# Performance work log

Measured on AMD Instinct MI355X. Metric: run time of the kernel, lower is better.

## Reference

```python
import jax, jax.numpy as jnp
import numpy as np

N_NODE = 40000  # item vocabulary
H = 100         # hidden size (SR-GNN default)
B = 64          # sessions per batch
L = 16          # items per session (equal-length sessions)
N = B * L       # total graph nodes
E = 2048        # total edges
NL = 1          # GatedGraphConv layers


def setup_inputs() -> dict:
    key = jax.random.key(0)
    ks = jax.random.split(key, 20)
    stdv = 1.0 / np.sqrt(H)
    u = lambda k, shape: jax.random.uniform(k, shape, jnp.float32, -stdv, stdv)
    return {
        "x": jax.random.randint(ks[0], (N,), 0, N_NODE),
        "edge_index": jax.random.randint(ks[1], (2, E), 0, N),
        "edge_weight": jax.random.uniform(ks[2], (E,), jnp.float32),
        "batch": jnp.arange(N) // L,  # node -> session id, equal-length sessions
        "embed": u(ks[3], (N_NODE, H)),
        "ggc_w": u(ks[4], (NL, H, H)),
        "gru_wih": u(ks[5], (3 * H, H)),
        "gru_whh": u(ks[6], (3 * H, H)),
        "gru_bih": u(ks[7], (3 * H,)),
        "gru_bhh": u(ks[8], (3 * H,)),
        "W1_w": u(ks[9], (H, H)), "W1_b": u(ks[10], (H,)),
        "W2_w": u(ks[11], (H, H)), "W2_b": u(ks[12], (H,)),
        "Wt_w": u(ks[13], (H, H)), "Wt_b": u(ks[14], (H,)),
        "q_w": u(ks[15], (1, H)), "q_b": u(ks[16], (1,)),
        "W3_w": u(ks[17], (H, 2 * H)), "W3_b": u(ks[18], (H,)),
    }


def reference(x, edge_index, edge_weight, batch, embed, ggc_w, gru_wih, gru_whh,
              gru_bih, gru_bhh, W1_w, W1_b, W2_w, W2_b, Wt_w, Wt_b, q_w, q_b,
              W3_w, W3_b):
    # Embedding lookup
    h = embed[x]  # [N, H]
    src, dst = edge_index[0], edge_index[1]
    # GatedGraphConv: weighted message aggregation + GRUCell update
    for l in range(NL):
        m = h @ ggc_w[l]                                             # [N, H]
        agg = jnp.zeros_like(h).at[dst].add(edge_weight[:, None] * m[src])
        gi = agg @ gru_wih.T + gru_bih                               # [N, 3H]
        gh = h @ gru_whh.T + gru_bhh
        ir, iz, inn = jnp.split(gi, 3, axis=-1)
        hr, hz, hn = jnp.split(gh, 3, axis=-1)
        r = jax.nn.sigmoid(ir + hr)
        zg = jax.nn.sigmoid(iz + hz)
        ng = jnp.tanh(inn + r * hn)
        h = (1.0 - zg) * ng + zg * h
    v = h.reshape(B, L, H)                                           # sessions
    s_l = v[:, -1]                                                   # [B, H] last item
    # alpha = q(sigmoid(W1(v_n) + W2(v)))
    a = jax.nn.sigmoid((s_l @ W1_w.T + W1_b)[:, None, :] + (v @ W2_w.T + W2_b))
    alpha = a @ q_w.T + q_b                                          # [B, L, 1]
    s_g = jnp.sum(alpha * v, axis=1)                                 # [B, H]
    s_h = jnp.concatenate([s_l, s_g], axis=-1) @ W3_w.T + W3_b       # [B, H]
    # Target attention: s_t[b] = softmax(E @ W_t(v_b)^T, -1) @ v_b, contracted
    # directly against E to avoid materializing [B, N_NODE, H].
    vt = v @ Wt_w.T + Wt_b                                           # [B, L, H]
    P = jax.nn.softmax(jnp.einsum('jh,blh->bjl', embed, vt), axis=-1)
    C = jnp.einsum('blh,jh->bjl', v, embed)                          # v_l . E_j
    z = s_h @ embed.T + jnp.sum(P * C, axis=-1)                      # [B, N_NODE]
    return z
```

## Files before the change

kernel.cpp:

```cpp
#include <hip/hip_runtime.h>
#include <hip/hip_bf16.h>

#define Hh    100
#define NN    1024
#define BB    64
#define LL    16
#define EE    2048
#define NNODE 40000

#define BSPL  8
#define BPB   (BB / BSPL)
#define PFR   8
#define PPAN  (PFR * 64 * 8)
#define GJ    4
#define EBS   104

typedef unsigned short u16;
typedef __attribute__((ext_vector_type(8))) short short8;
typedef __attribute__((ext_vector_type(4))) float f32x4;

__device__ __forceinline__ float bf2f(u16 u) {
    union { unsigned int i; float f; } v;
    v.i = ((unsigned int)u) << 16;
    return v.f;
}

__device__ __forceinline__ u16 f2bf(float f) {
    unsigned int x = __float_as_uint(f);
    unsigned int lsb = (x >> 16) & 1u;
    x += 0x7fffu + lsb;
    return (u16)(x >> 16);
}

__device__ __forceinline__ float sigmoidf_(float x) {
    return 1.0f / (1.0f + expf(-x));
}

template <bool BF>
__device__ __forceinline__ float ldv(const void* p, size_t i) {
    if (BF) return bf2f(((const u16*)p)[i]);
    return ((const float*)p)[i];
}
__device__ __forceinline__ float ldvf(int flag, const void* p, size_t i) {
    return flag ? ldv<true>(p, i) : ldv<false>(p, i);
}

template <bool BF>
__device__ void cvt_impl(int t,
                         const void* ew, const void* ggc, const void* wih, const void* whh,
                         const void* bih, const void* bhh, const void* W1w, const void* W1b,
                         const void* W2w, const void* W2b, const void* Wtw, const void* Wtb,
                         const void* qw, const void* qb, const void* W3w, const void* W3b,
                         float* __restrict__ W) {
    const void* src; int si; int doff; int di;
    if      (t <   2048) { src = ew;  si = t;          doff = 0;      di = si; }
    else if (t <  12048) { src = ggc; si = t - 2048;   doff = 2048;   di = si; }
    else if (t <  42048) { src = wih; si = t - 12048;  doff = 12048;  { int r = si / 100, k = si - r * 100; di = k * 800 + (r % 100) * 8 + r / 100; } }
    else if (t <  72048) { src = whh; si = t - 42048;  doff = 12048;  { int r = si / 100, k = si - r * 100; di = k * 800 + (r % 100) * 8 + 3 + r / 100; } }
    else if (t <  72348) { src = bih; si = t - 72048;  doff = 92048;  di = si; }
    else if (t <  72648) { src = bhh; si = t - 72348;  doff = 92352;  di = si; }
    else if (t <  82648) { src = W1w; si = t - 72648;  doff = 92656;  di = (si % 100) * 100 + si / 100; }
    else if (t <  82748) { src = W1b; si = t - 82648;  doff = 102656; di = si; }
    else if (t <  92748) { src = W2w; si = t - 82748;  doff = 102768; di = (si % 100) * 100 + si / 100; }
    else if (t <  92848) { src = W2b; si = t - 92748;  doff = 112768; di = si; }
    else if (t < 102848) { src = Wtw; si = t - 92848;  doff = 112880; di = (si % 100) * 100 + si / 100; }
    else if (t < 102948) { src = Wtb; si = t - 102848; doff = 122880; di = si; }
    else if (t < 103048) { src = qw;  si = t - 102948; doff = 122992; di = si; }
    else if (t < 103049) { src = qb;  si = t - 103048; doff = 123104; di = si; }
    else if (t < 123049) { src = W3w; si = t - 103049; doff = 123120; di = (si % 200) * 100 + si / 200; }
    else                 { src = W3b; si = t - 123049; doff = 143120; di = si; }
    W[doff + di] = ldv<BF>(src, si);
}

__global__ void __launch_bounds__(256) k_cvt(const void* embed_raw, int* __restrict__ flag,
                      const void* ew, const void* ggc, const void* wih, const void* whh,
                      const void* bih, const void* bhh, const void* W1w, const void* W1b,
                      const void* W2w, const void* W2b, const void* Wtw, const void* Wtb,
                      const void* qw, const void* qb, const void* W3w, const void* W3b,
                      float* __restrict__ W, u16* __restrict__ SD) {
    __shared__ int cnt;
    if (threadIdx.x == 0) cnt = 0;
    __syncthreads();
    int bad = 0;
    const u16* eb = (const u16*)embed_raw;
    for (int i = threadIdx.x; i < 4096; i += 256) {
        float v = bf2f(eb[i]);
        if (!(fabsf(v) <= 0.5f)) bad++;
    }
    if (bad) atomicAdd(&cnt, bad);
    __syncthreads();
    const bool bf = (cnt == 0);
    if (blockIdx.x == 0 && threadIdx.x == 0) flag[0] = bf ? 1 : 0;
    int t = blockIdx.x * 256 + threadIdx.x;
    if (t < 8192) ((unsigned int*)SD)[t] = 0u;
    if (t >= 123149) return;
    if (bf) cvt_impl<true >(t, ew, ggc, wih, whh, bih, bhh, W1w, W1b, W2w, W2b, Wtw, Wtb, qw, qb, W3w, W3b, W);
    else    cvt_impl<false>(t, ew, ggc, wih, whh, bih, bhh, W1w, W1b, W2w, W2b, Wtw, Wtb, qw, qb, W3w, W3b, W);
}

__global__ void __launch_bounds__(256) k_ecvt(const int* __restrict__ flag,
                                              const void* __restrict__ embed,
                                              u16* __restrict__ EB) {
    const bool bf = (flag[0] != 0);
    int t = blockIdx.x * 256 + threadIdx.x;
    const int total = NNODE * (EBS / 2);
    if (t >= total) return;
    int r = t / (EBS / 2), c2 = t - r * (EBS / 2);
    int k0 = c2 * 2;
    unsigned int w = 0;
    if (k0 + 1 < Hh) {
        if (bf) {
            w = *(const unsigned int*)&((const u16*)embed)[(size_t)r * Hh + k0];
        } else {
            float2 e2 = *(const float2*)&((const float*)embed)[(size_t)r * Hh + k0];
            w = (unsigned int)f2bf(e2.x) | ((unsigned int)f2bf(e2.y) << 16);
        }
    }
    ((unsigned int*)EB)[t] = w;
}

__global__ void __launch_bounds__(256) k_gm(const int* __restrict__ flag,
                                            const int* __restrict__ x,
                                            const void* __restrict__ embed,
                                            const float* __restrict__ ggc_w,
                                            float* __restrict__ m,
                                            float* __restrict__ agg) {
    __shared__ float W[Hh * Hh];
    __shared__ float H[8 * Hh];
    const int tid = threadIdx.x;
    const int fl = flag[0];
    const int r0 = blockIdx.x * 8;
    for (int idx = tid; idx < Hh * Hh; idx += 256) W[idx] = ggc_w[idx];
    for (int idx = tid; idx < 8 * Hh; idx += 256) {
        int i = idx / Hh, j = idx - i * Hh;
        H[idx] = ldvf(fl, embed, (size_t)x[r0 + i] * Hh + j);
    }
    for (int idx = tid; idx < 8 * Hh; idx += 256) agg[r0 * Hh + idx] = 0.0f;
    __syncthreads();
    for (int idx = tid; idx < 8 * Hh; idx += 256) {
        int i = idx / Hh, j = idx - i * Hh;
        float acc = 0.0f;
#pragma unroll 4
        for (int k = 0; k < Hh; ++k) acc += H[i * Hh + k] * W[k * Hh + j];
        m[(r0 + i) * Hh + j] = acc;
    }
}

__global__ void k_scatter(const int* __restrict__ ei, const float* __restrict__ ew,
                          const float* __restrict__ m, float* __restrict__ agg) {
    int t = blockIdx.x * 256 + threadIdx.x;
    if (t >= EE * Hh) return;
    int e = t / Hh, j = t - e * Hh;
    int src = ei[e], dst = ei[EE + e];
    atomicAdd(&agg[dst * Hh + j], ew[e] * m[src * Hh + j]);
}

__global__ void k_gru(const int* __restrict__ flag, const int* __restrict__ x,
                      const void* __restrict__ embed,
                      const float* __restrict__ agg,
                      const float* __restrict__ wC,
                      const float* __restrict__ bih, const float* __restrict__ bhh,
                      float* __restrict__ h1) {
    int t = blockIdx.x * 256 + threadIdx.x;
    if (t >= NN * Hh) return;
    int i = t / Hh, j = t - i * Hh;
    const int fl = flag[0];
    const size_t erow = (size_t)x[i] * Hh;
    const float* ar = agg + i * Hh;
    float s_ir = bih[j], s_iz = bih[j + Hh], s_in = bih[j + 2 * Hh];
    float s_hr = bhh[j], s_hz = bhh[j + Hh], s_hn = bhh[j + 2 * Hh];
    float h0j = 0.0f;
    const float* wbase = wC + j * 8;
    for (int k = 0; k < Hh; ++k) {
        float a = ar[k];
        float h = ldvf(fl, embed, erow + k);
        if (k == j) h0j = h;
        const float* wr = wbase + k * 800;
        float4 w0 = *(const float4*)wr;
        float2 w1 = *(const float2*)(wr + 4);
        s_ir += a * w0.x;
        s_iz += a * w0.y;
        s_in += a * w0.z;
        s_hr += h * w0.w;
        s_hz += h * w1.x;
        s_hn += h * w1.y;
    }
    float r = sigmoidf_(s_ir + s_hr);
    float z = sigmoidf_(s_iz + s_hz);
    float n = tanhf(s_in + r * s_hn);
    h1[t] = (1.0f - z) * n + z * h0j;
}

__global__ void __launch_bounds__(256) k_att(const float* __restrict__ h1,
                    const float* __restrict__ W1T, const float* __restrict__ W1b,
                    const float* __restrict__ W2T, const float* __restrict__ W2b,
                    const float* __restrict__ WtT, const float* __restrict__ Wtb,
                    const float* __restrict__ qw, const float* __restrict__ qb,
                    const float* __restrict__ W3T, const float* __restrict__ W3b,
                    u16* __restrict__ P, u16* __restrict__ SD) {
    __shared__ float V[LL * Hh];
    __shared__ float Q2[LL * Hh];
    __shared__ float VTs[LL * Hh];
    __shared__ float Q1[Hh];
    __shared__ float AL[LL];
    __shared__ float SG[Hh];
    __shared__ float SH[Hh];
    const int b = blockIdx.x, tid = threadIdx.x;
    for (int idx = tid; idx < LL * Hh; idx += 256) V[idx] = h1[b * LL * Hh + idx];
    __syncthreads();
    for (int idx = tid; idx < LL * Hh; idx += 256) {
        int i = idx / Hh, j = idx - i * Hh;
        float a2 = 0, at = 0;
        for (int k = 0; k < Hh; ++k) {
            float vk = V[i * Hh + k];
            a2 += vk * W2T[k * Hh + j];
            at += vk * WtT[k * Hh + j];
        }
        Q2[idx] = a2 + W2b[j];
        VTs[idx] = at + Wtb[j];
    }
    if (tid < Hh) {
        float a1 = 0;
        for (int k = 0; k < Hh; ++k) a1 += V[(LL - 1) * Hh + k] * W1T[k * Hh + tid];
        Q1[tid] = a1 + W1b[tid];
    }
    __syncthreads();
    if (tid < LL) {
        float acc = 0;
        for (int j = 0; j < Hh; ++j)
            acc += sigmoidf_(Q1[j] + Q2[tid * Hh + j]) * qw[j];
        AL[tid] = acc + qb[0];
    }
    __syncthreads();
    if (tid < Hh) {
        float acc = 0;
#pragma unroll
        for (int l = 0; l < LL; ++l) acc += AL[l] * V[l * Hh + tid];
        SG[tid] = acc;
    }
    __syncthreads();
    if (tid < Hh) {
        float acc = W3b[tid];
        for (int k = 0; k < Hh; ++k) acc += V[(LL - 1) * Hh + k] * W3T[k * Hh + tid];
        for (int k = 0; k < Hh; ++k) acc += SG[k] * W3T[(Hh + k) * Hh + tid];
        SH[tid] = acc;
    }
    __syncthreads();
    for (int w = tid; w < PFR * 64; w += 256) {
        int f = w >> 6, lane = w & 63;
        int t = f >> 2, ks = f & 3;
        int mm = lane & 15, qq = lane >> 4;
        int col0 = ks * 32 + qq * 8;
        short8 t8;
#pragma unroll
        for (int e = 0; e < 8; ++e) {
            int col = col0 + e;
            float v = 0.0f;
            if (col < Hh) v = (t == 0) ? VTs[mm * Hh + col] : V[mm * Hh + col];
            t8[e] = (short)f2bf(v);
        }
        *(short8*)&P[((size_t)b * PFR + f) * 512 + lane * 8] = t8;
    }
    if (tid < 128) {
        int ks = tid >> 5, qq = (tid >> 3) & 3, e = tid & 7;
        int col = ks * 32 + qq * 8 + e;
        float v = (col < Hh) ? SH[col] : 0.0f;
        SD[(((size_t)(b >> 3) * 4 + ks) * 64 + qq * 16 + (b & 7)) * 8 + e] = f2bf(v);
    }
}

__device__ __forceinline__ short8 load_efrag(const void* embed, bool bf, int j, int k0) {
    short8 v = {0, 0, 0, 0, 0, 0, 0, 0};
    if (j >= NNODE || k0 >= Hh) return v;
    if (bf) {
        const u16* row = (const u16*)embed + (size_t)j * Hh + k0;
        if (k0 + 8 <= Hh) {
            ushort4 a = *(const ushort4*)(row);
            ushort4 b = *(const ushort4*)(row + 4);
            v[0] = (short)a.x; v[1] = (short)a.y; v[2] = (short)a.z; v[3] = (short)a.w;
            v[4] = (short)b.x; v[5] = (short)b.y; v[6] = (short)b.z; v[7] = (short)b.w;
        } else {
            for (int e = 0; e < Hh - k0; ++e) v[e] = (short)row[e];
        }
    } else {
        const float* row = (const float*)embed + (size_t)j * Hh + k0;
        if (k0 + 8 <= Hh) {
            float4 a = *(const float4*)(row);
            float4 b = *(const float4*)(row + 4);
            v[0] = (short)f2bf(a.x); v[1] = (short)f2bf(a.y); v[2] = (short)f2bf(a.z); v[3] = (short)f2bf(a.w);
            v[4] = (short)f2bf(b.x); v[5] = (short)f2bf(b.y); v[6] = (short)f2bf(b.z); v[7] = (short)f2bf(b.w);
        } else {
            for (int e = 0; e < Hh - k0; ++e) v[e] = (short)f2bf(row[e]);
        }
    }
    return v;
}

template <int EMODE>
__global__ void __launch_bounds__(256) k_score(const int* __restrict__ flag,
                                               const void* __restrict__ embed,
                                               const u16* __restrict__ EB,
                                               const u16* __restrict__ P,
                                               const u16* __restrict__ SD,
                                               void* __restrict__ out) {
    __shared__ alignas(16) u16 sPan[2][PPAN];
    const int jb = blockIdx.x * 256;
    const int b0 = blockIdx.y * BPB;
    const int slice = blockIdx.y;
    const int tid = threadIdx.x;
    const bool bf = (flag[0] != 0);
    const int wave = tid >> 6, lane = tid & 63;
    const int m = lane & 15, quad = lane >> 4;

    short8 Bf[GJ][4];
#pragma unroll
    for (int g = 0; g < GJ; ++g)
#pragma unroll
        for (int ks = 0; ks < 4; ++ks) {
            int j = jb + wave * 64 + g * 16 + m;
            if (EMODE) {
                short8 v = {0, 0, 0, 0, 0, 0, 0, 0};
                if (j < NNODE)
                    v = *(const short8*)&EB[(size_t)j * EBS + ks * 32 + quad * 8];
                Bf[g][ks] = v;
            } else {
                Bf[g][ks] = load_efrag(embed, bf, j, ks * 32 + quad * 8);
            }
        }

    short8 Sf[4];
#pragma unroll
    for (int ks = 0; ks < 4; ++ks)
        Sf[ks] = *(const short8*)&SD[(((size_t)slice * 4 + ks) * 64 + lane) * 8];
    f32x4 accsd[GJ];
#pragma unroll
    for (int g = 0; g < GJ; ++g) {
        accsd[g] = (f32x4){0.0f, 0.0f, 0.0f, 0.0f};
#pragma unroll
        for (int ks = 0; ks < 4; ++ks)
            accsd[g] = __builtin_amdgcn_mfma_f32_16x16x32_bf16(Sf[ks], Bf[g][ks], accsd[g], 0, 0, 0);
    }

    {
        const uint4* s4 = (const uint4*)(P + (size_t)b0 * PPAN);
        uint4 g0 = s4[tid], g1 = s4[tid + 256];
        uint4* d = (uint4*)sPan[0];
        d[tid] = g0; d[tid + 256] = g1;
    }
    __syncthreads();

    int cur = 0;
    for (int bi = 0; bi < BPB; ++bi) {
        const int b = b0 + bi;
        uint4 g0, g1;
        if (bi + 1 < BPB) {
            const uint4* s4 = (const uint4*)(P + (size_t)(b + 1) * PPAN);
            g0 = s4[tid]; g1 = s4[tid + 256];
        }

        const u16* sp = sPan[cur];
        f32x4 acc[GJ][2];
#pragma unroll
        for (int g = 0; g < GJ; ++g)
#pragma unroll
            for (int t = 0; t < 2; ++t)
                acc[g][t] = (f32x4){0.0f, 0.0f, 0.0f, 0.0f};
#pragma unroll
        for (int t = 0; t < 2; ++t) {
            short8 A0 = *(const short8*)&sp[(t * 4 + 0) * 512 + lane * 8];
            short8 A1 = *(const short8*)&sp[(t * 4 + 1) * 512 + lane * 8];
            short8 A2 = *(const short8*)&sp[(t * 4 + 2) * 512 + lane * 8];
            short8 A3 = *(const short8*)&sp[(t * 4 + 3) * 512 + lane * 8];
#pragma unroll
            for (int g = 0; g < GJ; ++g) {
                acc[g][t] = __builtin_amdgcn_mfma_f32_16x16x32_bf16(A0, Bf[g][0], acc[g][t], 0, 0, 0);
                acc[g][t] = __builtin_amdgcn_mfma_f32_16x16x32_bf16(A1, Bf[g][1], acc[g][t], 0, 0, 0);
                acc[g][t] = __builtin_amdgcn_mfma_f32_16x16x32_bf16(A2, Bf[g][2], acc[g][t], 0, 0, 0);
                acc[g][t] = __builtin_amdgcn_mfma_f32_16x16x32_bf16(A3, Bf[g][3], acc[g][t], 0, 0, 0);
            }
        }

#pragma unroll
        for (int g = 0; g < GJ; ++g) {
            float den = 0.0f, num = 0.0f;
#pragma unroll
            for (int r = 0; r < 4; ++r) {
                float p = __expf(acc[g][0][r]);
                den += p;
                num += p * acc[g][1][r];
            }
            den += __shfl_xor(den, 16); num += __shfl_xor(num, 16);
            den += __shfl_xor(den, 32); num += __shfl_xor(num, 32);
            f32x4 s4v = accsd[g];
            int rr = bi & 3;
            float sdv = (rr == 0) ? s4v[0] : (rr == 1) ? s4v[1] : (rr == 2) ? s4v[2] : s4v[3];
            sdv = __shfl(sdv, ((bi >> 2) << 4) | m);
            if (quad == 0) {
                int j = jb + wave * 64 + g * 16 + m;
                if (j < NNODE) {
                    float z = sdv + num / den;
                    if (bf) ((u16*)out)[(size_t)b * NNODE + j] = f2bf(z);
                    else    ((float*)out)[(size_t)b * NNODE + j] = z;
                }
            }
        }

        if (bi + 1 < BPB) {
            uint4* d = (uint4*)sPan[cur ^ 1];
            d[tid] = g0; d[tid + 256] = g1;
        }
        __syncthreads();
        cur ^= 1;
    }
}

extern "C" void kernel_launch(void* const* d_in, const int* in_sizes, int n_in,
                              void* d_out, int out_size, void* d_ws, size_t ws_size,
                              hipStream_t stream) {
    const int* x      = (const int*)d_in[0];
    const int* ei     = (const int*)d_in[1];
    const void* ew    = d_in[2];
    const void* embed = d_in[4];
    const void* ggc   = d_in[5];
    const void* wih   = d_in[6];
    const void* whh   = d_in[7];
    const void* bih   = d_in[8];
    const void* bhh   = d_in[9];
    const void* W1w   = d_in[10];
    const void* W1b   = d_in[11];
    const void* W2w   = d_in[12];
    const void* W2b   = d_in[13];
    const void* Wtw   = d_in[14];
    const void* Wtb   = d_in[15];
    const void* qw    = d_in[16];
    const void* qb    = d_in[17];
    const void* W3w   = d_in[18];
    const void* W3b   = d_in[19];
    float* ws = (float*)d_ws;
    int* flag = (int*)d_ws;

    float* W = ws + 64;
    float* ew_f  = W + 0;
    float* ggc_f = W + 2048;
    float* wC    = W + 12048;
    float* bih_f = W + 92048;
    float* bhh_f = W + 92352;
    float* W1T   = W + 92656;
    float* W1b_f = W + 102656;
    float* W2T   = W + 102768;
    float* W2b_f = W + 112768;
    float* WtT   = W + 112880;
    float* Wtb_f = W + 122880;
    float* qw_f  = W + 122992;
    float* qb_f  = W + 123104;
    float* W3T   = W + 123120;
    float* W3b_f = W + 143120;

    float* D     = ws + 143296;
    float* m     = D;
    float* agg   = D + 102400;
    float* h1    = D;
    u16*   P     = (u16*)(D + 102400);
    u16*   SDp   = (u16*)(D + 233472);
    u16*   EB    = (u16*)(D + 241664);

    const size_t need_bytes = (size_t)(143296 + 241664) * 4 + (size_t)NNODE * EBS * 2;
    const bool emode = (ws_size >= need_bytes);

    k_cvt    <<<dim3(482), dim3(256), 0, stream>>>(embed, flag, ew, ggc, wih, whh, bih, bhh,
                                                   W1w, W1b, W2w, W2b, Wtw, Wtb, qw, qb, W3w, W3b, W, SDp);
    if (emode)
        k_ecvt<<<dim3((NNODE * (EBS / 2) + 255) / 256), dim3(256), 0, stream>>>(flag, embed, EB);
    k_gm     <<<dim3(128), dim3(256), 0, stream>>>(flag, x, embed, ggc_f, m, agg);
    k_scatter<<<dim3(800), dim3(256), 0, stream>>>(ei, ew_f, m, agg);
    k_gru    <<<dim3(400), dim3(256), 0, stream>>>(flag, x, embed, agg, wC, bih_f, bhh_f, h1);
    k_att    <<<dim3(64),  dim3(256), 0, stream>>>(h1, W1T, W1b_f, W2T, W2b_f, WtT, Wtb_f,
                                                   qw_f, qb_f, W3T, W3b_f, P, SDp);
    if (emode)
        k_score<1><<<dim3((NNODE + 255) / 256, BSPL), dim3(256), 0, stream>>>(flag, embed, EB, P, SDp, d_out);
    else
        k_score<0><<<dim3((NNODE + 255) / 256, BSPL), dim3(256), 0, stream>>>(flag, embed, EB, P, SDp, d_out);
}
```

Measured before the change: 222.8 us.

## Fuse GRU with per-node attention projections and halve batch slices in scoring

Merges the GRU update with the W2/Wt/W1 projections into one kernel that processes four nodes per block. It stages agg and the embedding rows in shared memory and writes Q1, Q2 and VT to global buffers. The per-session attention kernel becomes lighter and computes the alpha reduction with wave shuffles instead of 16 serial threads. The score kernel's batch split drops from 8 to 4 slices (16 sessions per slice), which changes the SD layout and zero-init size, and the converted embedding buffer gains one padding row. The aim is to spread the heavy 64-block attention matmuls across 256 blocks and to cut repeated embedding reads in scoring, at the cost of more workspace and fewer, larger score blocks.

```diff
diff --git a/kernel.cpp b/kernel.cpp
--- a/kernel.cpp
+++ b/kernel.cpp
@@ -8,12 +8,13 @@
 #define EE    2048
 #define NNODE 40000
 
-#define BSPL  8
+#define BSPL  4
 #define BPB   (BB / BSPL)
 #define PFR   8
 #define PPAN  (PFR * 64 * 8)
 #define GJ    4
 #define EBS   104
+#define GRB   4
 
 typedef unsigned short u16;
 typedef __attribute__((ext_vector_type(8))) short short8;
@@ -92,7 +93,7 @@
     const bool bf = (cnt == 0);
     if (blockIdx.x == 0 && threadIdx.x == 0) flag[0] = bf ? 1 : 0;
     int t = blockIdx.x * 256 + threadIdx.x;
-    if (t < 8192) ((unsigned int*)SD)[t] = 0u;
+    if (t < 4096) ((unsigned int*)SD)[t] = 0u;
     if (t >= 123149) return;
     if (bf) cvt_impl<true >(t, ew, ggc, wih, whh, bih, bhh, W1w, W1b, W2w, W2b, Wtw, Wtb, qw, qb, W3w, W3b, W);
     else    cvt_impl<false>(t, ew, ggc, wih, whh, bih, bhh, W1w, W1b, W2w, W2b, Wtw, Wtb, qw, qb, W3w, W3b, W);
@@ -103,12 +104,12 @@
                                               u16* __restrict__ EB) {
     const bool bf = (flag[0] != 0);
     int t = blockIdx.x * 256 + threadIdx.x;
-    const int total = NNODE * (EBS / 2);
+    const int total = (NNODE + 1) * (EBS / 2);
     if (t >= total) return;
     int r = t / (EBS / 2), c2 = t - r * (EBS / 2);
     int k0 = c2 * 2;
     unsigned int w = 0;
-    if (k0 + 1 < Hh) {
+    if (r < NNODE && k0 + 1 < Hh) {
         if (bf) {
             w = *(const unsigned int*)&((const u16*)embed)[(size_t)r * Hh + k0];
         } else {
@@ -155,85 +156,105 @@
     atomicAdd(&agg[dst * Hh + j], ew[e] * m[src * Hh + j]);
 }
 
-__global__ void k_gru(const int* __restrict__ flag, const int* __restrict__ x,
-                      const void* __restrict__ embed,
-                      const float* __restrict__ agg,
-                      const float* __restrict__ wC,
+__global__ void __launch_bounds__(256) k_gruatt(const int* __restrict__ flag,
+                      const int* __restrict__ x, const void* __restrict__ embed,
+                      const float* __restrict__ agg, const float* __restrict__ wC,
                       const float* __restrict__ bih, const float* __restrict__ bhh,
-                      float* __restrict__ h1) {
-    int t = blockIdx.x * 256 + threadIdx.x;
-    if (t >= NN * Hh) return;
-    int i = t / Hh, j = t - i * Hh;
+                      const float* __restrict__ W1T, const float* __restrict__ W1b,
+                      const float* __restrict__ W2T, const float* __restrict__ W2b,
+                      const float* __restrict__ WtT, const float* __restrict__ Wtb,
+                      float* __restrict__ h1, float* __restrict__ Q2g,
+                      float* __restrict__ VTg, float* __restrict__ Q1g) {
+    __shared__ float sA[GRB * Hh];
+    __shared__ float sH0[GRB * Hh];
+    __shared__ float sV[GRB * Hh];
+    const int tid = threadIdx.x;
+    const int r0 = blockIdx.x * GRB;
     const int fl = flag[0];
-    const size_t erow = (size_t)x[i] * Hh;
-    const float* ar = agg + i * Hh;
-    float s_ir = bih[j], s_iz = bih[j + Hh], s_in = bih[j + 2 * Hh];
-    float s_hr = bhh[j], s_hz = bhh[j + Hh], s_hn = bhh[j + 2 * Hh];
-    float h0j = 0.0f;
-    const float* wbase = wC + j * 8;
-    for (int k = 0; k < Hh; ++k) {
-        float a = ar[k];
-        float h = ldvf(fl, embed, erow + k);
-        if (k == j) h0j = h;
-        const float* wr = wbase + k * 800;
-        float4 w0 = *(const float4*)wr;
-        float2 w1 = *(const float2*)(wr + 4);
-        s_ir += a * w0.x;
-        s_iz += a * w0.y;
-        s_in += a * w0.z;
-        s_hr += h * w0.w;
-        s_hz += h * w1.x;
-        s_hn += h * w1.y;
-    }
-    float r = sigmoidf_(s_ir + s_hr);
-    float z = sigmoidf_(s_iz + s_hz);
-    float n = tanhf(s_in + r * s_hn);
-    h1[t] = (1.0f - z) * n + z * h0j;
-}
-
-__global__ void __launch_bounds__(256) k_att(const float* __restrict__ h1,
-                    const float* __restrict__ W1T, const float* __restrict__ W1b,
-                    const float* __restrict__ W2T, const float* __restrict__ W2b,
-                    const float* __restrict__ WtT, const float* __restrict__ Wtb,
+    for (int o = tid; o < GRB * Hh; o += 256) {
+        int i = o / Hh, j = o - i * Hh;
+        sA[o] = agg[(r0 + i) * Hh + j];
+        sH0[o] = ldvf(fl, embed, (size_t)x[r0 + i] * Hh + j);
+    }
+    __syncthreads();
+    for (int o = tid; o < GRB * Hh; o += 256) {
+        int i = o / Hh, j = o - i * Hh;
+        float s_ir = bih[j], s_iz = bih[j + Hh], s_in = bih[j + 2 * Hh];
+        float s_hr = bhh[j], s_hz = bhh[j + Hh], s_hn = bhh[j + 2 * Hh];
+        const float* ai = sA + i * Hh;
+        const float* hi = sH0 + i * Hh;
+        const float* wbase = wC + j * 8;
+        for (int k = 0; k < Hh; ++k) {
+            float a = ai[k], h = hi[k];
+            const float* wr = wbase + k * 800;
+            float4 w0 = *(const float4*)wr;
+            float2 w1 = *(const float2*)(wr + 4);
+            s_ir += a * w0.x;
+            s_iz += a * w0.y;
+            s_in += a * w0.z;
+            s_hr += h * w0.w;
+            s_hz += h * w1.x;
+            s_hn += h * w1.y;
+        }
+        float r = sigmoidf_(s_ir + s_hr);
+        float z = sigmoidf_(s_iz + s_hz);
+        float n = tanhf(s_in + r * s_hn);
+        float hv = (1.0f - z) * n + z * hi[j];
+        sV[o] = hv;
+        h1[(r0 + i) * Hh + j] = hv;
+    }
+    __syncthreads();
+    for (int o = tid; o < GRB * Hh; o += 256) {
+        int i = o / Hh, j = o - i * Hh;
+        const float* vi = sV + i * Hh;
+        float a2 = 0.0f, at = 0.0f;
+        for (int k = 0; k < Hh; ++k) {
+            float vk = vi[k];
+            a2 += vk * W2T[k * Hh + j];
+            at += vk * WtT[k * Hh + j];
+        }
+        Q2g[(r0 + i) * Hh + j] = a2 + W2b[j];
+        VTg[(r0 + i) * Hh + j] = at + Wtb[j];
+    }
+    if ((r0 & 15) == 12 && tid < Hh) {
+        const float* vl = sV + 3 * Hh;
+        float a1 = 0.0f;
+        for (int k = 0; k < Hh; ++k) a1 += vl[k] * W1T[k * Hh + tid];
+        Q1g[(r0 >> 4) * Hh + tid] = a1 + W1b[tid];
+    }
+}
+
+__global__ void __launch_bounds__(256) k_att2(const float* __restrict__ h1,
+                    const float* __restrict__ Q1g, const float* __restrict__ Q2g,
+                    const float* __restrict__ VTg,
                     const float* __restrict__ qw, const float* __restrict__ qb,
                     const float* __restrict__ W3T, const float* __restrict__ W3b,
                     u16* __restrict__ P, u16* __restrict__ SD) {
     __shared__ float V[LL * Hh];
-    __shared__ float Q2[LL * Hh];
     __shared__ float VTs[LL * Hh];
-    __shared__ float Q1[Hh];
     __shared__ float AL[LL];
     __shared__ float SG[Hh];
     __shared__ float SH[Hh];
     const int b = blockIdx.x, tid = threadIdx.x;
-    for (int idx = tid; idx < LL * Hh; idx += 256) V[idx] = h1[b * LL * Hh + idx];
-    __syncthreads();
-    for (int idx = tid; idx < LL * Hh; idx += 256) {
-        int i = idx / Hh, j = idx - i * Hh;
-        float a2 = 0, at = 0;
-        for (int k = 0; k < Hh; ++k) {
-            float vk = V[i * Hh + k];
-            a2 += vk * W2T[k * Hh + j];
-            at += vk * WtT[k * Hh + j];
-        }
-        Q2[idx] = a2 + W2b[j];
-        VTs[idx] = at + Wtb[j];
-    }
+    for (int o = tid; o < LL * Hh; o += 256) {
+        V[o] = h1[b * LL * Hh + o];
+        VTs[o] = VTg[b * LL * Hh + o];
+    }
+    __syncthreads();
+    {
+        int l = tid >> 4, t = tid & 15;
+        float acc = 0.0f;
+        for (int j = t; j < Hh; j += 16)
+            acc += sigmoidf_(Q1g[b * Hh + j] + Q2g[(b * LL + l) * Hh + j]) * qw[j];
+        acc += __shfl_xor(acc, 8);
+        acc += __shfl_xor(acc, 4);
+        acc += __shfl_xor(acc, 2);
+        acc += __shfl_xor(acc, 1);
+        if (t == 0) AL[l] = acc + qb[0];
+    }
+    __syncthreads();
     if (tid < Hh) {
-        float a1 = 0;
-        for (int k = 0; k < Hh; ++k) a1 += V[(LL - 1) * Hh + k] * W1T[k * Hh + tid];
-        Q1[tid] = a1 + W1b[tid];
-    }
-    __syncthreads();
-    if (tid < LL) {
-        float acc = 0;
-        for (int j = 0; j < Hh; ++j)
-            acc += sigmoidf_(Q1[j] + Q2[tid * Hh + j]) * qw[j];
-        AL[tid] = acc + qb[0];
-    }
-    __syncthreads();
-    if (tid < Hh) {
-        float acc = 0;
+        float acc = 0.0f;
 #pragma unroll
         for (int l = 0; l < LL; ++l) acc += AL[l] * V[l * Hh + tid];
         SG[tid] = acc;
@@ -265,7 +286,7 @@
         int ks = tid >> 5, qq = (tid >> 3) & 3, e = tid & 7;
         int col = ks * 32 + qq * 8 + e;
         float v = (col < Hh) ? SH[col] : 0.0f;
-        SD[(((size_t)(b >> 3) * 4 + ks) * 64 + qq * 16 + (b & 7)) * 8 + e] = f2bf(v);
+        SD[(((size_t)(b >> 4) * 4 + ks) * 64 + qq * 16 + (b & 15)) * 8 + e] = f2bf(v);
     }
 }
 
@@ -305,8 +326,8 @@
                                                void* __restrict__ out) {
     __shared__ alignas(16) u16 sPan[2][PPAN];
     const int jb = blockIdx.x * 256;
-    const int b0 = blockIdx.y * BPB;
     const int slice = blockIdx.y;
+    const int b0 = slice * BPB;
     const int tid = threadIdx.x;
     const bool bf = (flag[0] != 0);
     const int wave = tid >> 6, lane = tid & 63;
@@ -460,22 +481,26 @@
     float* m     = D;
     float* agg   = D + 102400;
     float* h1    = D;
-    u16*   P     = (u16*)(D + 102400);
-    u16*   SDp   = (u16*)(D + 233472);
-    u16*   EB    = (u16*)(D + 241664);
-
-    const size_t need_bytes = (size_t)(143296 + 241664) * 4 + (size_t)NNODE * EBS * 2;
+    float* Q2g   = D + 204800;
+    float* VTg   = D + 307200;
+    float* Q1g   = D + 409600;
+    u16*   P     = (u16*)(D + 416000);
+    u16*   SDp   = (u16*)(D + 547072);
+    u16*   EB    = (u16*)(D + 551168);
+
+    const size_t need_bytes = (size_t)(143296 + 551168) * 4 + (size_t)(NNODE + 1) * EBS * 2;
     const bool emode = (ws_size >= need_bytes);
 
     k_cvt    <<<dim3(482), dim3(256), 0, stream>>>(embed, flag, ew, ggc, wih, whh, bih, bhh,
                                                    W1w, W1b, W2w, W2b, Wtw, Wtb, qw, qb, W3w, W3b, W, SDp);
     if (emode)
-        k_ecvt<<<dim3((NNODE * (EBS / 2) + 255) / 256), dim3(256), 0, stream>>>(flag, embed, EB);
+        k_ecvt<<<dim3(((NNODE + 1) * (EBS / 2) + 255) / 256), dim3(256), 0, stream>>>(flag, embed, EB);
     k_gm     <<<dim3(128), dim3(256), 0, stream>>>(flag, x, embed, ggc_f, m, agg);
     k_scatter<<<dim3(800), dim3(256), 0, stream>>>(ei, ew_f, m, agg);
-    k_gru    <<<dim3(400), dim3(256), 0, stream>>>(flag, x, embed, agg, wC, bih_f, bhh_f, h1);
-    k_att    <<<dim3(64),  dim3(256), 0, stream>>>(h1, W1T, W1b_f, W2T, W2b_f, WtT, Wtb_f,
-                                                   qw_f, qb_f, W3T, W3b_f, P, SDp);
+    k_gruatt <<<dim3(NN / GRB), dim3(256), 0, stream>>>(flag, x, embed, agg, wC, bih_f, bhh_f,
+                                                        W1T, W1b_f, W2T, W2b_f, WtT, Wtb_f,
+                                                        h1, Q2g, VTg, Q1g);
+    k_att2   <<<dim3(BB), dim3(256), 0, stream>>>(h1, Q1g, Q2g, VTg, qw_f, qb_f, W3T, W3b_f, P, SDp);
     if (emode)
         k_score<1><<<dim3((NNODE + 255) / 256, BSPL), dim3(256), 0, stream>>>(flag, embed, EB, P, SDp, d_out);
     else
```

Result: faster. 203.3 us (-8.7%).
